# Kernel tuning notes

Measured on AMD Instinct MI355X. Metric: run time of the kernel, lower is better.

Reference implementation:

```python
import jax, jax.numpy as jnp
import numpy as np

B, N, E = 4, 8192, 131072
NODE_F, EDGE_F, HID, ACT = 16, 1, 128, 8


def _glorot(key, shape):
    fan_in, fan_out = shape[0], shape[1]
    lim = np.sqrt(6.0 / (fan_in + fan_out))
    return jax.random.uniform(key, shape, jnp.float32, -lim, lim)


def setup_inputs() -> dict:
    key = jax.random.key(0)
    ks = jax.random.split(key, 20)
    inp = {
        'node_features': jax.random.randint(ks[0], (B, N, NODE_F), 0, 10, jnp.int32),
        'edge_index': jax.random.randint(ks[1], (B, 2, E), 0, N, jnp.int64),
        'edge_features': jax.random.normal(ks[2], (B, E, EDGE_F), jnp.float32),
        # conv1: in = 2*NODE_F + EDGE_F
        'c1_w1': _glorot(ks[3], (2 * NODE_F + EDGE_F, HID)), 'c1_b1': jnp.zeros((HID,), jnp.float32),
        'c1_w2': _glorot(ks[4], (HID, HID)), 'c1_b2': jnp.zeros((HID,), jnp.float32),
        # conv2/conv3: in = 2*HID + 1
        'c2_w1': _glorot(ks[5], (2 * HID + 1, HID)), 'c2_b1': jnp.zeros((HID,), jnp.float32),
        'c2_w2': _glorot(ks[6], (HID, HID)), 'c2_b2': jnp.zeros((HID,), jnp.float32),
        'c3_w1': _glorot(ks[7], (2 * HID + 1, HID)), 'c3_b1': jnp.zeros((HID,), jnp.float32),
        'c3_w2': _glorot(ks[8], (HID, HID)), 'c3_b2': jnp.zeros((HID,), jnp.float32),
        'lin_w': _glorot(ks[9], (NODE_F + HID, ACT)), 'lin_b': jnp.zeros((ACT,), jnp.float32),
    }
    return inp


def _edge_conv(x, src, dst, ea, w1, b1, w2, b2):
    # message: cat([x_i (target), x_j (source), edge_attr]) -> Linear -> LeakyReLU -> Linear
    m = jnp.concatenate([x[dst], x[src], ea], axis=1)          # [E, 2F+EF]
    m = jax.nn.leaky_relu(m @ w1 + b1) @ w2 + b2               # [E, out]
    out = jax.ops.segment_min(m, dst, num_segments=x.shape[0])  # min-aggregate at targets
    cnt = jnp.zeros((x.shape[0],), m.dtype).at[dst].add(1.0)
    return jnp.where(cnt[:, None] > 0, out, 0.0)                # nodes w/o in-edges -> 0 (PyG)


def _graph_fwd(x0, ei, ea, p):
    x0 = x0.astype(jnp.float32)  # torch casts to IntTensor then MLP promotes; math on integer values
    src, dst = ei[0], ei[1]      # flow='source_to_target'
    x = jax.nn.leaky_relu(_edge_conv(x0, src, dst, ea, p['c1_w1'], p['c1_b1'], p['c1_w2'], p['c1_b2']))
    x = jax.nn.leaky_relu(_edge_conv(x, src, dst, ea, p['c2_w1'], p['c2_b1'], p['c2_w2'], p['c2_b2']))
    x = jax.nn.leaky_relu(_edge_conv(x, src, dst, ea, p['c3_w1'], p['c3_b1'], p['c3_w2'], p['c3_b2']))
    x = jnp.concatenate([x0, x], axis=1)
    return jax.nn.softplus(x @ p['lin_w'] + p['lin_b'])         # [N, ACT]


def reference(node_features, edge_index, edge_features,
              c1_w1, c1_b1, c1_w2, c1_b2,
              c2_w1, c2_b1, c2_w2, c2_b2,
              c3_w1, c3_b1, c3_w2, c3_b2,
              lin_w, lin_b):
    p = dict(c1_w1=c1_w1, c1_b1=c1_b1, c1_w2=c1_w2, c1_b2=c1_b2,
             c2_w1=c2_w1, c2_b1=c2_b1, c2_w2=c2_w2, c2_b2=c2_b2,
             c3_w1=c3_w1, c3_b1=c3_b1, c3_w2=c3_w2, c3_b2=c3_b2,
             lin_w=lin_w, lin_b=lin_b)
    return jax.vmap(lambda x, ei, ea: _graph_fwd(x, ei, ea, p))(
        node_features, edge_index, edge_features)               # [B, N, ACT]
```

## Files before the change

### kernel.cpp

```cpp
#include <hip/hip_runtime.h>

#define B_ 4
#define N_ 8192
#define E_ 131072
#define HID_ 128

typedef unsigned short us8 __attribute__((ext_vector_type(8)));
typedef unsigned short us4 __attribute__((ext_vector_type(4)));
typedef unsigned int   ui4 __attribute__((ext_vector_type(4)));
typedef int            i4  __attribute__((ext_vector_type(4)));
typedef __bf16         v8bf __attribute__((ext_vector_type(8)));
typedef float          v4f  __attribute__((ext_vector_type(4)));
typedef float          v2f  __attribute__((ext_vector_type(2)));

#define KEY_INF 0xFF800000u

__device__ __forceinline__ float b2f(unsigned short u) {
    return __uint_as_float(((unsigned)u) << 16);
}
__device__ __forceinline__ unsigned short f2b(float f) {
    unsigned x = __float_as_uint(f);
    return (unsigned short)((x + 0x7fffu + ((x >> 16) & 1u)) >> 16);
}
__device__ __forceinline__ unsigned fkey(float f) {
    unsigned b = __float_as_uint(f);
    return (b & 0x80000000u) ? ~b : (b | 0x80000000u);
}
__device__ __forceinline__ float funkey(unsigned k) {
    unsigned b = (k & 0x80000000u) ? (k ^ 0x80000000u) : ~k;
    return __uint_as_float(b);
}

__device__ __forceinline__ void repack_one(const float* __restrict__ w1, const float* __restrict__ w2,
                                           unsigned short* __restrict__ w1n, unsigned short* __restrict__ w2t,
                                           int F, int KPAD, int gid) {
    int t1 = 256 * KPAD;
    if (gid < t1) {
        int j = gid / KPAD, k = gid - j * KPAD;
        float v = 0.f;
        if (k < F) v = (j < 128) ? w1[k * 128 + j] : w1[(F + k) * 128 + (j - 128)];
        w1n[gid] = f2b(v);
    } else {
        int g = gid - t1;
        if (g < 16384) { int j = g >> 7, k = g & 127; w2t[g] = f2b(w2[k * 128 + j]); }
    }
}

__global__ void k_setup(const int* __restrict__ nf, unsigned short* __restrict__ x0b,
                        unsigned* __restrict__ cnt, unsigned* __restrict__ agg,
                        const float* __restrict__ w1a, const float* __restrict__ w2a,
                        const float* __restrict__ w1b, const float* __restrict__ w2b,
                        const float* __restrict__ w1c, const float* __restrict__ w2c,
                        unsigned short* __restrict__ w1n0, unsigned short* __restrict__ w2t0,
                        unsigned short* __restrict__ w1n1, unsigned short* __restrict__ w2t1,
                        unsigned short* __restrict__ w1n2, unsigned short* __restrict__ w2t2) {
    const int bid = blockIdx.x, tid = threadIdx.x;
    if (bid >= 4096) {
        const int rb = bid - 4096;
        const int gid = rb * 256 + tid;
        if (rb < 96)       repack_one(w1a, w2a, w1n0, w2t0, 16, 32, gid);
        else if (rb < 288) repack_one(w1b, w2b, w1n1, w2t1, 128, 128, gid - 96 * 256);
        else               repack_one(w1c, w2c, w1n2, w2t2, 128, 128, gid - 288 * 256);
        return;
    }
    const int gid = bid * 256 + tid;
    ui4 v = {KEY_INF, KEY_INF, KEY_INF, KEY_INF};
    ((ui4*)agg)[gid] = v;
    if (bid < 512) {
        i4 x = ((const i4*)nf)[gid];
        us4 o;
        o[0] = f2b((float)x[0]); o[1] = f2b((float)x[1]);
        o[2] = f2b((float)x[2]); o[3] = f2b((float)x[3]);
        ((us4*)x0b)[gid] = o;
    }
    if (bid < 128) cnt[gid] = 0u;
}

__global__ void k_hist(const int* __restrict__ ei, unsigned* __restrict__ cnt) {
    int gid = blockIdx.x * 256 + threadIdx.x;
    int b = gid >> 17, e = gid & (E_ - 1);
    int dst = ei[(b << 18) + E_ + e];
    atomicAdd(&cnt[(b << 13) + dst], 1u);
}

__global__ void k_scan(unsigned* __restrict__ cnt) {
    int b = blockIdx.x;
    __shared__ unsigned ps[256];
    unsigned* c = cnt + (b << 13) + threadIdx.x * 32;
    unsigned loc[32]; unsigned s = 0;
#pragma unroll
    for (int i = 0; i < 32; i++) { loc[i] = c[i]; s += loc[i]; }
    ps[threadIdx.x] = s;
    __syncthreads();
    for (int off = 1; off < 256; off <<= 1) {
        unsigned v = (threadIdx.x >= (unsigned)off) ? ps[threadIdx.x - off] : 0u;
        __syncthreads();
        ps[threadIdx.x] += v;
        __syncthreads();
    }
    unsigned run = ps[threadIdx.x] - s;
#pragma unroll
    for (int i = 0; i < 32; i++) { c[i] = run; run += loc[i]; }
}

__global__ void k_scatter(const int* __restrict__ ei, unsigned* __restrict__ wptr,
                          int* __restrict__ perm) {
    int gid = blockIdx.x * 256 + threadIdx.x;
    int b = gid >> 17, e = gid & (E_ - 1);
    int dst = ei[(b << 18) + E_ + e];
    unsigned pos = atomicAdd(&wptr[(b << 13) + dst], 1u);
    perm[(b << 17) + pos] = e;
}

template<int KPAD, bool FROM_AGG>
__global__ __launch_bounds__(256, 3) void k_node(
    const unsigned short* __restrict__ xin,
    unsigned* __restrict__ agg,
    const unsigned short* __restrict__ w1n,
    const float* __restrict__ bias1,
    unsigned short* __restrict__ Yd,
    unsigned short* __restrict__ Ys)
{
    constexpr int ASTR = KPAD + 8;
    __shared__ __align__(16) unsigned short A[64 * ASTR];
    __shared__ __align__(16) unsigned short Yb[64 * 264];

    const int tid = threadIdx.x;
    const int wave = tid >> 6, lane = tid & 63, lq = lane >> 4, lm = lane & 15;
    const int tile = (blockIdx.x & 7) * 64 + (blockIdx.x >> 3);
    const int n0 = tile * 64;

    v8bf wf[4][KPAD / 32]; float b1v[4];
#pragma unroll
    for (int nt = 0; nt < 4; nt++) {
        const int col = wave * 64 + nt * 16 + lm;
#pragma unroll
        for (int ks = 0; ks < KPAD / 32; ks++)
            wf[nt][ks] = *(const v8bf*)&w1n[col * KPAD + ks * 32 + lq * 8];
        b1v[nt] = (col < 128) ? bias1[col] : 0.f;
    }

    {
        const int row = tid >> 2, p = tid & 3;
        if (FROM_AGG) {
#pragma unroll
            for (int i = 0; i < 8; i++) {
                const int c = p + 4 * i;
                unsigned* ap = agg + ((size_t)(n0 + row)) * 128 + c * 4;
                ui4 k = *(ui4*)ap;
                ui4 inf = {KEY_INF, KEY_INF, KEY_INF, KEY_INF};
                *(ui4*)ap = inf;
                us4 o;
#pragma unroll
                for (int j = 0; j < 4; j++) {
                    float v = (k[j] == KEY_INF) ? 0.f : funkey(k[j]);
                    v = (v > 0.f) ? v : 0.01f * v;
                    o[j] = f2b(v);
                }
                *(us4*)&A[row * ASTR + c * 4] = o;
            }
        } else {
            us4 v = *(const us4*)(xin + ((size_t)(n0 + row)) * 16 + p * 4);
            *(us4*)&A[row * ASTR + p * 4] = v;
            us4 z = {0, 0, 0, 0};
            *(us4*)&A[row * ASTR + 16 + p * 4] = z;
        }
    }
    __syncthreads();

#pragma unroll
    for (int mt = 0; mt < 4; mt++) {
        v4f acc[4];
#pragma unroll
        for (int nt = 0; nt < 4; nt++) acc[nt] = v4f{0.f, 0.f, 0.f, 0.f};
#pragma unroll
        for (int ks = 0; ks < KPAD / 32; ks++) {
            v8bf a = *(const v8bf*)&A[(mt * 16 + lm) * ASTR + ks * 32 + lq * 8];
#pragma unroll
            for (int nt = 0; nt < 4; nt++)
                acc[nt] = __builtin_amdgcn_mfma_f32_16x16x32_bf16(a, wf[nt][ks], acc[nt], 0, 0, 0);
        }
#pragma unroll
        for (int nt = 0; nt < 4; nt++) {
            const int col = wave * 64 + nt * 16 + lm;
#pragma unroll
            for (int r = 0; r < 4; r++)
                Yb[(mt * 16 + lq * 4 + r) * 264 + col] = f2b(acc[nt][r] + b1v[nt]);
        }
    }
    __syncthreads();

    const int bb = tile >> 7, nl0 = (tile & 127) * 64;
#pragma unroll
    for (int i = 0; i < 8; i++) {
        const int idx = tid + 256 * i;
        const int row = idx >> 5, c = idx & 31;
        us8 v = *(const us8*)&Yb[row * 264 + c * 8];
        const int col0 = c * 8;
        unsigned short* dp = (col0 < 128)
            ? (Yd + ((size_t)(bb * N_) + nl0 + row) * 128 + col0)
            : (Ys + ((size_t)(bb * N_) + nl0 + row) * 128 + (col0 - 128));
        *(us8*)dp = v;
    }
}

__global__ __launch_bounds__(256, 4) void k_edge(
    const unsigned short* __restrict__ Yd,
    const unsigned short* __restrict__ Ys,
    const int* __restrict__ ei,
    const float* __restrict__ eaf,
    const int* __restrict__ perm,
    const unsigned short* __restrict__ w2t,
    const float* __restrict__ weap,
    const float* __restrict__ bias2,
    unsigned* __restrict__ agg)
{
    __shared__ __align__(16) unsigned short Hs[128 * 136];
    __shared__ __align__(16) int   dstl[128];
    __shared__ __align__(16) float weal[128];

    const int tid = threadIdx.x;
    const int wave = tid >> 6, lane = tid & 63, lq = lane >> 4, lm = lane & 15;

    if (tid < 128) weal[tid] = weap[tid];

    v8bf w2f[2][4]; float b2v[2];
#pragma unroll
    for (int nt = 0; nt < 2; nt++) {
        const int col = wave * 32 + nt * 16 + lm;
#pragma unroll
        for (int ks = 0; ks < 4; ks++)
            w2f[nt][ks] = *(const v8bf*)&w2t[col * 128 + ks * 32 + lq * 8];
        b2v[nt] = bias2[col];
    }
    __syncthreads();

    const int arow = tid >> 1, p = tid & 1;
    const int s = ((arow & 0x70) >> 2) | ((arow & 0x0C) << 3) | (arow & 3);

    int t = (blockIdx.x & 7) * 512 + (blockIdx.x >> 3);
    int b = t >> 10;
    int e = perm[(b << 17) + (t & 1023) * 128 + s];
    int src = ei[(b << 18) + e];
    int dst = ei[(b << 18) + E_ + e];
    float ea = eaf[(b << 17) + e];
    const ui4* ydp = (const ui4*)(Yd + ((size_t)(b * N_) + dst) * 128);
    const ui4* ysp = (const ui4*)(Ys + ((size_t)(b * N_) + src) * 128);
    ui4 va0 = ydp[p], vb0 = ysp[p];

    for (int jj = 0; jj < 4; jj++) {
        const int curb = b;
        if (p == 0) dstl[s] = dst;

        {
            const v2f eav2 = {ea, ea};
            const v2f c01  = {0.01f, 0.01f};
            ui4 va = va0, vb = vb0;
#pragma unroll
            for (int i = 0; i < 8; i++) {
                ui4 na, nb;
                if (i < 7) { na = ydp[p + 2 * (i + 1)]; nb = ysp[p + 2 * (i + 1)]; }
                const int c = p + 2 * i;
                ui4 od;
#pragma unroll
                for (int k = 0; k < 4; k++) {
                    v2f a, bb2, z;
                    a[0]   = __uint_as_float(va[k] << 16);
                    a[1]   = __uint_as_float(va[k] & 0xffff0000u);
                    bb2[0] = __uint_as_float(vb[k] << 16);
                    bb2[1] = __uint_as_float(vb[k] & 0xffff0000u);
                    v2f wv = *(const v2f*)&weal[c * 8 + 2 * k];
                    z = a + bb2 + wv * eav2;
                    z = __builtin_elementwise_max(z, z * c01);
                    od[k] = __builtin_amdgcn_perm(__float_as_uint(z[1]) + 0x8000u,
                                                  __float_as_uint(z[0]) + 0x8000u,
                                                  0x07060302u);
                }
                *(ui4*)&Hs[arow * 136 + c * 8] = od;
                va = na; vb = nb;
            }
        }
        __syncthreads();

        t += 128;
        if (jj < 3) {
            b = t >> 10;
            e = perm[(b << 17) + (t & 1023) * 128 + s];
            src = ei[(b << 18) + e];
            dst = ei[(b << 18) + E_ + e];
            ea = eaf[(b << 17) + e];
            ydp = (const ui4*)(Yd + ((size_t)(b * N_) + dst) * 128);
            ysp = (const ui4*)(Ys + ((size_t)(b * N_) + src) * 128);
            va0 = ydp[p]; vb0 = ysp[p];
        }

        {
            const int col0 = wave * 32 + lm, col1 = col0 + 16;
            unsigned* aggb = agg + (size_t)(curb * N_) * 128;
            float cur0 = 0.f, cur1 = 0.f; int curd = -1;
#pragma unroll
            for (int mt = 0; mt < 8; mt++) {
                v4f acc0 = {b2v[0], b2v[0], b2v[0], b2v[0]};
                v4f acc1 = {b2v[1], b2v[1], b2v[1], b2v[1]};
#pragma unroll
                for (int ks = 0; ks < 4; ks++) {
                    v8bf a = *(const v8bf*)&Hs[(mt * 16 + lm) * 136 + ks * 32 + lq * 8];
                    acc0 = __builtin_amdgcn_mfma_f32_16x16x32_bf16(a, w2f[0][ks], acc0, 0, 0, 0);
                    acc1 = __builtin_amdgcn_mfma_f32_16x16x32_bf16(a, w2f[1][ks], acc1, 0, 0, 0);
                }
                i4 dv = *(const i4*)&dstl[lq * 32 + mt * 4];
#pragma unroll
                for (int r = 0; r < 4; r++) {
                    const float v0 = acc0[r];
                    const float v1 = acc1[r];
                    const int d = dv[r];
                    if (d != curd) {
                        if (curd >= 0) {
                            atomicMin(aggb + (size_t)curd * 128 + col0, fkey(cur0));
                            atomicMin(aggb + (size_t)curd * 128 + col1, fkey(cur1));
                        }
                        curd = d; cur0 = v0; cur1 = v1;
                    } else {
                        cur0 = fminf(cur0, v0); cur1 = fminf(cur1, v1);
                    }
                }
            }
            atomicMin(aggb + (size_t)curd * 128 + col0, fkey(cur0));
            atomicMin(aggb + (size_t)curd * 128 + col1, fkey(cur1));
        }
        __syncthreads();
    }
}

__global__ __launch_bounds__(256, 4) void k_final(
    const unsigned short* __restrict__ x0b, const unsigned* __restrict__ agg,
    const float* __restrict__ lw, const float* __restrict__ lb,
    float* __restrict__ out) {
    __shared__ float w[144 * 8];
    __shared__ float bias8[8];
    __shared__ float xs[64 * 129];
    const int tid = threadIdx.x;
    for (int i = tid; i < 1152; i += 256) w[i] = lw[i];
    if (tid < 8) bias8[tid] = lb[tid];
    const int n0 = blockIdx.x * 64;
#pragma unroll
    for (int i = 0; i < 8; i++) {
        const int idx = tid + 256 * i;
        const int row = idx >> 5, c = idx & 31;
        ui4 k = ((const ui4*)(agg + ((size_t)(n0 + row)) * 128))[c];
#pragma unroll
        for (int j = 0; j < 4; j++) {
            float v = (k[j] == KEY_INF) ? 0.f : funkey(k[j]);
            v = fmaxf(v, 0.01f * v);
            xs[row * 129 + c * 4 + j] = v;
        }
    }
    __syncthreads();
    const int node = tid >> 2, ap = (tid & 3) * 2;
    float a0 = bias8[ap], a1 = bias8[ap + 1];
    const unsigned short* x0 = x0b + (size_t)(n0 + node) * 16;
#pragma unroll
    for (int f = 0; f < 16; f++) {
        const float xv = b2f(x0[f]);
        a0 += xv * w[f * 8 + ap]; a1 += xv * w[f * 8 + ap + 1];
    }
    const float* xr = &xs[node * 129];
#pragma unroll 8
    for (int f = 0; f < 128; f++) {
        const float xv = xr[f];
        a0 += xv * w[(16 + f) * 8 + ap]; a1 += xv * w[(16 + f) * 8 + ap + 1];
    }
    v2f o;
    o[0] = fmaxf(a0, 0.f) + log1pf(expf(-fabsf(a0)));
    o[1] = fmaxf(a1, 0.f) + log1pf(expf(-fabsf(a1)));
    *(v2f*)&out[(size_t)(n0 + node) * 8 + ap] = o;
}

extern "C" void kernel_launch(void* const* d_in, const int* in_sizes, int n_in,
                              void* d_out, int out_size, void* d_ws, size_t ws_size,
                              hipStream_t stream) {
    (void)in_sizes; (void)n_in; (void)out_size; (void)ws_size;
    const int* nf  = (const int*)d_in[0];
    const int* ei  = (const int*)d_in[1];
    const float* eaf = (const float*)d_in[2];
    const float* cw1[3] = {(const float*)d_in[3],  (const float*)d_in[7],  (const float*)d_in[11]};
    const float* cb1[3] = {(const float*)d_in[4],  (const float*)d_in[8],  (const float*)d_in[12]};
    const float* cw2[3] = {(const float*)d_in[5],  (const float*)d_in[9],  (const float*)d_in[13]};
    const float* cb2[3] = {(const float*)d_in[6],  (const float*)d_in[10], (const float*)d_in[14]};
    const float* lw = (const float*)d_in[15];
    const float* lb = (const float*)d_in[16];
    float* out = (float*)d_out;

    size_t off = 0;
    auto carve = [&](size_t bytes) { void* p = (char*)d_ws + off; off += (bytes + 255) & ~(size_t)255; return p; };
    unsigned short* x0b  = (unsigned short*)carve((size_t)B_ * N_ * 16 * 2);
    unsigned*       agg  = (unsigned*)carve((size_t)B_ * N_ * 128 * 4);
    unsigned*       cnt  = (unsigned*)carve((size_t)B_ * N_ * 4);
    int*            perm = (int*)carve((size_t)B_ * E_ * 4);
    unsigned short* Yd   = (unsigned short*)carve((size_t)B_ * N_ * 128 * 2);
    unsigned short* Ys   = (unsigned short*)carve((size_t)B_ * N_ * 128 * 2);
    unsigned short* w1n0 = (unsigned short*)carve(256 * 32 * 2);
    unsigned short* w2t0 = (unsigned short*)carve(128 * 128 * 2);
    unsigned short* w1n1 = (unsigned short*)carve(256 * 128 * 2);
    unsigned short* w2t1 = (unsigned short*)carve(128 * 128 * 2);
    unsigned short* w1n2 = (unsigned short*)carve(256 * 128 * 2);
    unsigned short* w2t2 = (unsigned short*)carve(128 * 128 * 2);

    k_setup<<<4576, 256, 0, stream>>>(nf, x0b, cnt, agg,
                                      cw1[0], cw2[0], cw1[1], cw2[1], cw1[2], cw2[2],
                                      w1n0, w2t0, w1n1, w2t1, w1n2, w2t2);
    k_hist<<<2048, 256, 0, stream>>>(ei, cnt);
    k_scan<<<B_, 256, 0, stream>>>(cnt);
    k_scatter<<<2048, 256, 0, stream>>>(ei, cnt, perm);

    k_node<32, false><<<512, 256, 0, stream>>>(x0b, agg, w1n0, cb1[0], Yd, Ys);
    k_edge<<<1024, 256, 0, stream>>>(Yd, Ys, ei, eaf, perm, w2t0, cw1[0] + 32 * 128, cb2[0], agg);

    k_node<128, true><<<512, 256, 0, stream>>>(x0b, agg, w1n1, cb1[1], Yd, Ys);
    k_edge<<<1024, 256, 0, stream>>>(Yd, Ys, ei, eaf, perm, w2t1, cw1[1] + 256 * 128, cb2[1], agg);

    k_node<128, true><<<512, 256, 0, stream>>>(x0b, agg, w1n2, cb1[2], Yd, Ys);
    k_edge<<<1024, 256, 0, stream>>>(Yd, Ys, ei, eaf, perm, w2t2, cw1[2] + 256 * 128, cb2[2], agg);

    k_final<<<512, 256, 0, stream>>>(x0b, agg, lw, lb, out);
}
```

Before: 316.8 us.

## Retile edge MFMA to 64x64 per wave, swizzle LDS, widen scan block

k_edge now has each wave compute a 64-row by 64-column output tile, up from 128 rows by 32 columns. Each A fragment read from LDS therefore feeds four MFMAs instead of two, which halves LDS reads per MFMA. The padded Hs layout is replaced by an XOR swizzle to avoid bank conflicts, and the gather loads use a triple-buffered prefetch two steps ahead in place of the cross-iteration prefetch. k_scan moves to 1024 threads per block. Costs are more registers for the B fragments and accumulators, the loss of the next-batch row prefetch that overlapped the MFMA phase, and fewer rows per wave for the min run-merging, which can mean more atomics.

```diff
diff --git a/kernel.cpp b/kernel.cpp
--- a/kernel.cpp
+++ b/kernel.cpp
@@ -83,16 +83,16 @@
     atomicAdd(&cnt[(b << 13) + dst], 1u);
 }
 
-__global__ void k_scan(unsigned* __restrict__ cnt) {
+__global__ __launch_bounds__(1024) void k_scan(unsigned* __restrict__ cnt) {
     int b = blockIdx.x;
-    __shared__ unsigned ps[256];
-    unsigned* c = cnt + (b << 13) + threadIdx.x * 32;
-    unsigned loc[32]; unsigned s = 0;
-#pragma unroll
-    for (int i = 0; i < 32; i++) { loc[i] = c[i]; s += loc[i]; }
+    __shared__ unsigned ps[1024];
+    unsigned* c = cnt + (b << 13) + threadIdx.x * 8;
+    unsigned loc[8]; unsigned s = 0;
+#pragma unroll
+    for (int i = 0; i < 8; i++) { loc[i] = c[i]; s += loc[i]; }
     ps[threadIdx.x] = s;
     __syncthreads();
-    for (int off = 1; off < 256; off <<= 1) {
+    for (int off = 1; off < 1024; off <<= 1) {
         unsigned v = (threadIdx.x >= (unsigned)off) ? ps[threadIdx.x - off] : 0u;
         __syncthreads();
         ps[threadIdx.x] += v;
@@ -100,7 +100,7 @@
     }
     unsigned run = ps[threadIdx.x] - s;
 #pragma unroll
-    for (int i = 0; i < 32; i++) { c[i] = run; run += loc[i]; }
+    for (int i = 0; i < 8; i++) { c[i] = run; run += loc[i]; }
 }
 
 __global__ void k_scatter(const int* __restrict__ ei, unsigned* __restrict__ wptr,
@@ -215,19 +215,21 @@
     const float* __restrict__ bias2,
     unsigned* __restrict__ agg)
 {
-    __shared__ __align__(16) unsigned short Hs[128 * 136];
+    __shared__ __align__(16) unsigned short Hs[128 * 128];
     __shared__ __align__(16) int   dstl[128];
     __shared__ __align__(16) float weal[128];
 
     const int tid = threadIdx.x;
     const int wave = tid >> 6, lane = tid & 63, lq = lane >> 4, lm = lane & 15;
+    const int h = wave >> 1;
+    const int colbase = (wave & 1) * 64 + lm;
 
     if (tid < 128) weal[tid] = weap[tid];
 
-    v8bf w2f[2][4]; float b2v[2];
-#pragma unroll
-    for (int nt = 0; nt < 2; nt++) {
-        const int col = wave * 32 + nt * 16 + lm;
+    v8bf w2f[4][4]; float b2v[4];
+#pragma unroll
+    for (int nt = 0; nt < 4; nt++) {
+        const int col = colbase + nt * 16;
 #pragma unroll
         for (int ks = 0; ks < 4; ks++)
             w2f[nt][ks] = *(const v8bf*)&w2t[col * 128 + ks * 32 + lq * 8];
@@ -236,7 +238,8 @@
     __syncthreads();
 
     const int arow = tid >> 1, p = tid & 1;
-    const int s = ((arow & 0x70) >> 2) | ((arow & 0x0C) << 3) | (arow & 3);
+    const int s = (arow & 0x43) | ((arow & 0x30) >> 2) | ((arow & 0x0C) << 2);
+    const int rsw = arow & 15;
 
     int t = (blockIdx.x & 7) * 512 + (blockIdx.x >> 3);
     int b = t >> 10;
@@ -244,31 +247,33 @@
     int src = ei[(b << 18) + e];
     int dst = ei[(b << 18) + E_ + e];
     float ea = eaf[(b << 17) + e];
-    const ui4* ydp = (const ui4*)(Yd + ((size_t)(b * N_) + dst) * 128);
-    const ui4* ysp = (const ui4*)(Ys + ((size_t)(b * N_) + src) * 128);
-    ui4 va0 = ydp[p], vb0 = ysp[p];
 
     for (int jj = 0; jj < 4; jj++) {
         const int curb = b;
         if (p == 0) dstl[s] = dst;
 
         {
+            const ui4* ydp = (const ui4*)(Yd + ((size_t)(curb * N_) + dst) * 128);
+            const ui4* ysp = (const ui4*)(Ys + ((size_t)(curb * N_) + src) * 128);
             const v2f eav2 = {ea, ea};
             const v2f c01  = {0.01f, 0.01f};
-            ui4 va = va0, vb = vb0;
+            ui4 va[3], vb[3];
+            va[0] = ydp[p];     vb[0] = ysp[p];
+            va[1] = ydp[p + 2]; vb[1] = ysp[p + 2];
 #pragma unroll
             for (int i = 0; i < 8; i++) {
-                ui4 na, nb;
-                if (i < 7) { na = ydp[p + 2 * (i + 1)]; nb = ysp[p + 2 * (i + 1)]; }
+                if (i < 6) { va[(i + 2) % 3] = ydp[p + 2 * (i + 2)];
+                             vb[(i + 2) % 3] = ysp[p + 2 * (i + 2)]; }
+                const ui4 cva = va[i % 3], cvb = vb[i % 3];
                 const int c = p + 2 * i;
                 ui4 od;
 #pragma unroll
                 for (int k = 0; k < 4; k++) {
                     v2f a, bb2, z;
-                    a[0]   = __uint_as_float(va[k] << 16);
-                    a[1]   = __uint_as_float(va[k] & 0xffff0000u);
-                    bb2[0] = __uint_as_float(vb[k] << 16);
-                    bb2[1] = __uint_as_float(vb[k] & 0xffff0000u);
+                    a[0]   = __uint_as_float(cva[k] << 16);
+                    a[1]   = __uint_as_float(cva[k] & 0xffff0000u);
+                    bb2[0] = __uint_as_float(cvb[k] << 16);
+                    bb2[1] = __uint_as_float(cvb[k] & 0xffff0000u);
                     v2f wv = *(const v2f*)&weal[c * 8 + 2 * k];
                     z = a + bb2 + wv * eav2;
                     z = __builtin_elementwise_max(z, z * c01);
@@ -276,8 +281,8 @@
                                                   __float_as_uint(z[0]) + 0x8000u,
                                                   0x07060302u);
                 }
-                *(ui4*)&Hs[arow * 136 + c * 8] = od;
-                va = na; vb = nb;
+                *(ui4*)&Hs[arow * 128 + (c ^ rsw) * 8] = od;
+                va[i % 3] = va[i % 3];
             }
         }
         __syncthreads();
@@ -289,44 +294,49 @@
             src = ei[(b << 18) + e];
             dst = ei[(b << 18) + E_ + e];
             ea = eaf[(b << 17) + e];
-            ydp = (const ui4*)(Yd + ((size_t)(b * N_) + dst) * 128);
-            ysp = (const ui4*)(Ys + ((size_t)(b * N_) + src) * 128);
-            va0 = ydp[p]; vb0 = ysp[p];
         }
 
         {
-            const int col0 = wave * 32 + lm, col1 = col0 + 16;
             unsigned* aggb = agg + (size_t)(curb * N_) * 128;
-            float cur0 = 0.f, cur1 = 0.f; int curd = -1;
-#pragma unroll
-            for (int mt = 0; mt < 8; mt++) {
-                v4f acc0 = {b2v[0], b2v[0], b2v[0], b2v[0]};
-                v4f acc1 = {b2v[1], b2v[1], b2v[1], b2v[1]};
+            float cur[4]; int curd = -1;
+#pragma unroll
+            for (int nt = 0; nt < 4; nt++) cur[nt] = 0.f;
+#pragma unroll
+            for (int mt = 0; mt < 4; mt++) {
+                const int row = h * 64 + mt * 16 + lm;
+                v4f acc[4];
+#pragma unroll
+                for (int nt = 0; nt < 4; nt++)
+                    acc[nt] = v4f{b2v[nt], b2v[nt], b2v[nt], b2v[nt]};
 #pragma unroll
                 for (int ks = 0; ks < 4; ks++) {
-                    v8bf a = *(const v8bf*)&Hs[(mt * 16 + lm) * 136 + ks * 32 + lq * 8];
-                    acc0 = __builtin_amdgcn_mfma_f32_16x16x32_bf16(a, w2f[0][ks], acc0, 0, 0, 0);
-                    acc1 = __builtin_amdgcn_mfma_f32_16x16x32_bf16(a, w2f[1][ks], acc1, 0, 0, 0);
+                    v8bf a = *(const v8bf*)&Hs[row * 128 + (((ks * 4 + lq) ^ lm) * 8)];
+#pragma unroll
+                    for (int nt = 0; nt < 4; nt++)
+                        acc[nt] = __builtin_amdgcn_mfma_f32_16x16x32_bf16(a, w2f[nt][ks], acc[nt], 0, 0, 0);
                 }
-                i4 dv = *(const i4*)&dstl[lq * 32 + mt * 4];
+                i4 dv = *(const i4*)&dstl[h * 64 + lq * 16 + mt * 4];
 #pragma unroll
                 for (int r = 0; r < 4; r++) {
-                    const float v0 = acc0[r];
-                    const float v1 = acc1[r];
                     const int d = dv[r];
                     if (d != curd) {
                         if (curd >= 0) {
-                            atomicMin(aggb + (size_t)curd * 128 + col0, fkey(cur0));
-                            atomicMin(aggb + (size_t)curd * 128 + col1, fkey(cur1));
+#pragma unroll
+                            for (int nt = 0; nt < 4; nt++)
+                                atomicMin(aggb + (size_t)curd * 128 + colbase + nt * 16, fkey(cur[nt]));
                         }
-                        curd = d; cur0 = v0; cur1 = v1;
+                        curd = d;
+#pragma unroll
+                        for (int nt = 0; nt < 4; nt++) cur[nt] = acc[nt][r];
                     } else {
-                        cur0 = fminf(cur0, v0); cur1 = fminf(cur1, v1);
+#pragma unroll
+                        for (int nt = 0; nt < 4; nt++) cur[nt] = fminf(cur[nt], acc[nt][r]);
                     }
                 }
             }
-            atomicMin(aggb + (size_t)curd * 128 + col0, fkey(cur0));
-            atomicMin(aggb + (size_t)curd * 128 + col1, fkey(cur1));
+#pragma unroll
+            for (int nt = 0; nt < 4; nt++)
+                atomicMin(aggb + (size_t)curd * 128 + colbase + nt * 16, fkey(cur[nt]));
         }
         __syncthreads();
     }
@@ -410,7 +420,7 @@
                                       cw1[0], cw2[0], cw1[1], cw2[1], cw1[2], cw2[2],
                                       w1n0, w2t0, w1n1, w2t1, w1n2, w2t2);
     k_hist<<<2048, 256, 0, stream>>>(ei, cnt);
-    k_scan<<<B_, 256, 0, stream>>>(cnt);
+    k_scan<<<B_, 1024, 0, stream>>>(cnt);
     k_scatter<<<2048, 256, 0, stream>>>(ei, cnt, perm);
 
     k_node<32, false><<<512, 256, 0, stream>>>(x0b, agg, w1n0, cb1[0], Yd, Ys);
```

Measured after the change: 410.8 us. 29.7% more time.
